# Optimization experiments

Hardware: AMD Instinct MI355X
Metric: run time of the kernel (lower is better)

Reference implementation:

```python
import jax, jax.numpy as jnp
import numpy as np
from jax import lax

L = 50      # observation_len
P = 30      # pred_len
N = 2048    # num nearby obstacles
EMB = 64    # embed_size
NH = 128    # node_hidden_size
EH = 256    # edge_hidden_size
AD = 64     # attention_dim
CNN = 2048  # resnet50 fc.in_features


def setup_inputs() -> dict:
    key = jax.random.key(0)
    ks = jax.random.split(key, 20)
    def rn(k, shape, s=1.0):
        return jax.random.normal(k, shape, jnp.float32) * s
    w = 0.05
    return {
        "img_embedding": rn(ks[0], (1, CNN)),
        "target_obs_pos": rn(ks[1], (1, L, 2)),
        "target_obs_pos_rel": rn(ks[2], (1, L, 2)),
        "nearby_obs_pos": rn(ks[3], (1, N, L, 2)),
        "nearby_obs_pos_rel": rn(ks[4], (1, N, L, 2)),
        "nearby_obs_hist_sizes": jax.random.randint(ks[5], (1, N, 1), 0, L + 1),
        "target_obs_hist_size": L,
        "target_h0": rn(ks[6], (NH,), w),
        "target_c0": rn(ks[7], (NH,), w),
        "W_temb": rn(ks[8], (2, EMB), w), "b_temb": jnp.zeros((EMB,), jnp.float32),
        "Wih_t": rn(ks[9], (EMB, 4 * NH), w), "Whh_t": rn(ks[10], (NH, 4 * NH), w),
        "bih_t": jnp.zeros((4 * NH,), jnp.float32), "bhh_t": jnp.zeros((4 * NH,), jnp.float32),
        "W_tatt": rn(ks[11], (2, AD), w), "b_tatt": jnp.zeros((AD,), jnp.float32),
        "nearby_h0": rn(ks[12], (EH,), w),
        "nearby_c0": rn(ks[13], (EH,), w),
        "W_nemb": rn(ks[14], (2, EMB), w), "b_nemb": jnp.zeros((EMB,), jnp.float32),
        "Wih_n": rn(ks[15], (EMB, 4 * EH), w), "Whh_n": rn(ks[16], (EH, 4 * EH), w),
        "bih_n": jnp.zeros((4 * EH,), jnp.float32), "bhh_n": jnp.zeros((4 * EH,), jnp.float32),
        "W_natt": rn(ks[17], (2, AD), w), "b_natt": jnp.zeros((AD,), jnp.float32),
        "W_pred": rn(ks[18], (NH + CNN + EH, 2), w), "b_pred": jnp.zeros((2,), jnp.float32),
    }


def _lstm_cell(x, h, c, Wih, Whh, bih, bhh, H):
    # PyTorch LSTM gate order: i, f, g, o
    g = x @ Wih + h @ Whh + bih + bhh
    i = jax.nn.sigmoid(g[..., :H])
    f = jax.nn.sigmoid(g[..., H:2 * H])
    gg = jnp.tanh(g[..., 2 * H:3 * H])
    o = jax.nn.sigmoid(g[..., 3 * H:])
    c2 = f * c + i * gg
    return o * jnp.tanh(c2), c2


def _forward(img_embedding, target_obs_pos, target_obs_pos_rel, nearby_obs_pos,
             nearby_obs_pos_rel, target_h0, target_c0, W_temb, b_temb,
             Wih_t, Whh_t, bih_t, bhh_t, W_tatt, b_tatt,
             nearby_h0, nearby_c0, W_nemb, b_nemb,
             Wih_n, Whh_n, bih_n, bhh_n, W_natt, b_natt,
             W_pred, b_pred, nearby_obs_hist_sizes, target_obs_hist_size):
    nhist = nearby_obs_hist_sizes.reshape(N)
    inv_sqrt_d = 1.0 / jnp.sqrt(jnp.float32(AD))

    def attention(trel, tpos, npos, nh, nmask, Ht_prev):
        # scores scaled by curr_N / sqrt(attention_dim), softmax over masked nearby.
        # max-subtracted softmax is mathematically identical to the original exp/sum.
        currN = jnp.sum(nmask.astype(jnp.float32))
        an = (tpos - npos) @ W_natt + b_natt          # [N, AD]
        at = trel @ W_tatt + b_tatt                   # [AD]
        scores = (an @ at) * currN * inv_sqrt_d       # [N]
        w = jax.nn.softmax(jnp.where(nmask, scores, -1e30))
        return jnp.where(currN >= 1.0, w @ nh, Ht_prev)

    def obs_step(carry, x):
        th, tc, nh, nc, Ht = carry
        t, tpos, trel, npos, nrel = x
        tmask = target_obs_hist_size > (L - t)
        nmask = nhist > (L - t)
        th2, tc2 = _lstm_cell(trel @ W_temb + b_temb, th, tc, Wih_t, Whh_t, bih_t, bhh_t, NH)
        th = jnp.where(tmask, th2, th)
        tc = jnp.where(tmask, tc2, tc)
        nh2, nc2 = _lstm_cell(nrel @ W_nemb + b_nemb, nh, nc, Wih_n, Whh_n, bih_n, bhh_n, EH)
        m = nmask[:, None]
        nh = jnp.where(m, nh2, nh)
        nc = jnp.where(m, nc2, nc)
        Ht = attention(trel, tpos, npos, nh, nmask, Ht)
        return (th, tc, nh, nc, Ht), None

    np_tm = jnp.swapaxes(nearby_obs_pos[0], 0, 1)      # [L, N, 2] time-major
    nr_tm = jnp.swapaxes(nearby_obs_pos_rel[0], 0, 1)
    xs = (jnp.arange(1, L), target_obs_pos[0, 1:], target_obs_pos_rel[0, 1:],
          np_tm[1:], nr_tm[1:])
    init = (target_h0, target_c0,
            jnp.broadcast_to(nearby_h0, (N, EH)),
            jnp.broadcast_to(nearby_c0, (N, EH)),
            nearby_h0)
    (th, tc, nh, nc, Ht), _ = lax.scan(obs_step, init, xs)

    # During prediction the original reuses nearby pos/rel from the last obs step.
    npos_last = nearby_obs_pos[0, :, L - 1, :]
    nrel_last = nearby_obs_pos_rel[0, :, L - 1, :]
    xn_last = nrel_last @ W_nemb + b_nemb
    all_mask = jnp.ones((N,), bool)

    def pred_step(carry, _):
        th, tc, nh, nc, Ht, pos = carry
        pred = jnp.concatenate([th, img_embedding[0], Ht]) @ W_pred + b_pred  # [2]
        pos = pos + pred
        th, tc = _lstm_cell(pred @ W_temb + b_temb, th, tc, Wih_t, Whh_t, bih_t, bhh_t, NH)
        nh, nc = _lstm_cell(xn_last, nh, nc, Wih_n, Whh_n, bih_n, bhh_n, EH)
        Ht = attention(pred, pos, npos_last, nh, all_mask, Ht)
        return (th, tc, nh, nc, Ht, pos), pred

    carry0 = (th, tc, nh, nc, Ht, target_obs_pos[0, L - 1])
    _, preds = lax.scan(pred_step, carry0, None, length=P)
    return preds[None]                                 # [1, P, 2]


def reference(img_embedding, target_obs_pos, target_obs_pos_rel, nearby_obs_pos,
              nearby_obs_pos_rel, nearby_obs_hist_sizes, target_obs_hist_size,
              target_h0, target_c0, W_temb, b_temb, Wih_t, Whh_t, bih_t, bhh_t,
              W_tatt, b_tatt, nearby_h0, nearby_c0, W_nemb, b_nemb,
              Wih_n, Whh_n, bih_n, bhh_n, W_natt, b_natt, W_pred, b_pred):
    return _forward(img_embedding, target_obs_pos, target_obs_pos_rel, nearby_obs_pos,
                    nearby_obs_pos_rel, target_h0, target_c0, W_temb, b_temb,
                    Wih_t, Whh_t, bih_t, bhh_t, W_tatt, b_tatt,
                    nearby_h0, nearby_c0, W_nemb, b_nemb,
                    Wih_n, Whh_n, bih_n, bhh_n, W_natt, b_natt,
                    W_pred, b_pred, nearby_obs_hist_sizes, target_obs_hist_size)
```

## Files before the change

### kernel.cpp

```cpp
#include <hip/hip_runtime.h>
#include <hip/hip_bf16.h>
#include <cstdint>

#define LH   50
#define PP   30
#define NAG  2048
#define NHID 128
#define EHID 256
#define ADIM 64
#define CNND 2048

typedef __attribute__((ext_vector_type(8))) short bf16x8;
typedef __attribute__((ext_vector_type(4))) float f32x4;

enum : int {
  WS_WT  = 0,
  WS_WHT = 131072,
  WS_WFN = 163840,
  WS_BFN = 165888,
  WS_WFT = 166912,
  WS_BFT = 167936,
  WS_TH  = 168448,
  WS_TC  = 168576,
  WS_W49 = 168704,
  WS_CN  = 170752,
  WS_Z   = 170756,
  WS_FLG = 293636,
  WS_HG  = 293892,
  WS_END = 556036
};

__device__ __forceinline__ float sigf(float x){ return 1.0f/(1.0f + __expf(-x)); }
__device__ __forceinline__ float tanhfast(float x){
  x = fminf(15.0f, fmaxf(-15.0f, x));
  float e = __expf(2.0f*x);
  return (e - 1.0f)/(e + 1.0f);
}
__device__ __forceinline__ float bfs(short s){
  return __uint_as_float(((unsigned)(unsigned short)s) << 16);
}
__device__ __forceinline__ void ast(unsigned* p, unsigned v){
  __hip_atomic_store(p, v, __ATOMIC_RELAXED, __HIP_MEMORY_SCOPE_AGENT);
}
__device__ __forceinline__ unsigned ald(const unsigned* p){
  return __hip_atomic_load(p, __ATOMIC_RELAXED, __HIP_MEMORY_SCOPE_AGENT);
}

__global__ void k_prep(const float* __restrict__ Whhn, const float* __restrict__ Whht,
                       const float* __restrict__ Wnemb, const float* __restrict__ bnemb,
                       const float* __restrict__ Wihn,  const float* __restrict__ bihn,
                       const float* __restrict__ bhhn,
                       const float* __restrict__ Wtemb, const float* __restrict__ btemb,
                       const float* __restrict__ Wiht,  const float* __restrict__ biht,
                       const float* __restrict__ bhht,
                       const float* __restrict__ trel,  const int* __restrict__ thsp,
                       const float* __restrict__ th0,   const float* __restrict__ tc0,
                       const float* __restrict__ tpos,  const float* __restrict__ npos,
                       const int* __restrict__ nhist,
                       const float* __restrict__ Wtatt, const float* __restrict__ btatt,
                       const float* __restrict__ Wnatt, const float* __restrict__ bnatt,
                       float* __restrict__ ws)
{
  __shared__ float ps[2304];
  const int b = blockIdx.x, tid = threadIdx.x;
  if (b < 256){
    float (*t)[33] = (float(*)[33])ps;
    __hip_bfloat16* WT = (__hip_bfloat16*)(ws + WS_WT);
    const int tx = tid & 31, ty = tid >> 5;
    const int j0 = (b & 31) << 5;
    const int c  = b >> 5;
    const int e0 = c << 5;
    #pragma unroll
    for (int r = 0; r < 4; ++r)
      t[ty + 8*r][tx] = Whhn[(e0 + ty + 8*r)*1024 + j0 + tx];
    __syncthreads();
    #pragma unroll
    for (int r = 0; r < 4; ++r)
      WT[c*32768 + r*8192 + (j0 + tx)*8 + ty] = __float2bfloat16(t[ty + 8*r][tx]);
  } else if (b == 256){
    for (int j = tid; j < 1024; j += 256){
      float a0=0.f, a1=0.f, ab=0.f;
      for (int k=0;k<64;k++){
        const float w = Wihn[k*1024 + j];
        a0 += Wnemb[k]*w; a1 += Wnemb[64+k]*w; ab += bnemb[k]*w;
      }
      ws[WS_WFN + j]        = a0;
      ws[WS_WFN + 1024 + j] = a1;
      ws[WS_BFN + j]        = ab + bihn[j] + bhhn[j];
    }
    for (int j = tid; j < 512; j += 256){
      float a0=0.f, a1=0.f, ab=0.f;
      for (int k=0;k<64;k++){
        const float w = Wiht[k*512 + j];
        a0 += Wtemb[k]*w; a1 += Wtemb[64+k]*w; ab += btemb[k]*w;
      }
      ws[WS_WFT + j]       = a0;
      ws[WS_WFT + 512 + j] = a1;
      ws[WS_BFT + j]       = ab + biht[j] + bhht[j];
    }
    __hip_bfloat16* WTt = (__hip_bfloat16*)(ws + WS_WHT);
    for (int j = tid; j < 512; j += 256)
      for (int k = 0; k < 128; ++k)
        WTt[j*128 + k] = __float2bfloat16(Whht[k*512 + j]);
    ast((unsigned*)(ws + WS_FLG) + tid, 0u);
  } else if (b == 257){
    float* hT  = ps;
    float* cT  = ps + 128;
    float* gT  = ps + 256;
    float* wfa = ps + 768;
    float* wfb = ps + 1280;
    float* bfT = ps + 1792;
    #pragma unroll
    for (int q = 0; q < 2; ++q){
      const int j = tid + q*256;
      float a0=0.f, a1=0.f, ab=0.f;
      for (int k=0;k<64;k++){
        const float w = Wiht[k*512 + j];
        a0 += Wtemb[k]*w; a1 += Wtemb[64+k]*w; ab += btemb[k]*w;
      }
      wfa[j] = a0; wfb[j] = a1; bfT[j] = ab + biht[j] + bhht[j];
    }
    if (tid < 128){ hT[tid] = th0[tid]; cT[tid] = tc0[tid]; }
    __syncthreads();
    const int ths = thsp[0];
    int t0 = 51 - ths; if (t0 < 1) t0 = 1;
    for (int t = t0; t < 50; ++t){
      const float x0 = trel[2*t], x1 = trel[2*t+1];
      #pragma unroll
      for (int q = 0; q < 2; ++q){
        const int j = tid + q*256;
        float acc = x0*wfa[j] + x1*wfb[j] + bfT[j];
        for (int k = 0; k < 128; ++k) acc += hT[k]*Whht[k*512 + j];
        gT[j] = acc;
      }
      __syncthreads();
      if (tid < 128){
        const float ig = sigf(gT[tid]),          fg = sigf(gT[128 + tid]);
        const float gg = tanhfast(gT[256 + tid]), og = sigf(gT[384 + tid]);
        const float c2 = fg*cT[tid] + ig*gg;
        cT[tid] = c2; hT[tid] = og*tanhfast(c2);
      }
      __syncthreads();
    }
    if (tid < 128){ ws[WS_TH + tid] = hT[tid]; ws[WS_TC + tid] = cT[tid]; }
  } else {
    float* at  = ps;
    float* red = ps + 64;
    float* uv  = ps + 320;
    const int t = LH - 1;
    const float tr0 = trel[2*t], tr1 = trel[2*t+1];
    const float tp0 = tpos[2*t], tp1 = tpos[2*t+1];
    if (tid < ADIM) at[tid] = tr0*Wtatt[tid] + tr1*Wtatt[ADIM+tid] + btatt[tid];
    int cnt = 0;
    #pragma unroll
    for (int i = 0; i < 8; ++i) cnt += (nhist[tid + 256*i] > (LH - t)) ? 1 : 0;
    red[tid] = (float)cnt;
    __syncthreads();
    if (tid == 0){
      float u0=0.f,u1=0.f,v=0.f;
      for (int k=0;k<ADIM;k++){ u0 += Wnatt[k]*at[k]; u1 += Wnatt[ADIM+k]*at[k]; v += bnatt[k]*at[k]; }
      uv[0]=u0; uv[1]=u1; uv[2]=v;
    }
    for (int s = 128; s > 0; s >>= 1){ if (tid < s) red[tid] += red[tid+s]; __syncthreads(); }
    const float currN = red[0];
    __syncthreads();
    const float u0 = uv[0], u1 = uv[1], v = uv[2];
    const float scale = currN * 0.125f;
    float sc[8]; float smax = -3.0e38f;
    #pragma unroll
    for (int i = 0; i < 8; ++i){
      const int n = tid + 256*i;
      const float p0 = npos[n*100 + 2*t], p1 = npos[n*100 + 2*t + 1];
      float s = scale * ((tp0-p0)*u0 + (tp1-p1)*u1 + v);
      s = (nhist[n] > (LH - t)) ? s : -1.0e30f;
      sc[i] = s; smax = fmaxf(smax, s);
    }
    red[tid] = smax; __syncthreads();
    for (int s = 128; s > 0; s >>= 1){ if (tid<s) red[tid] = fmaxf(red[tid], red[tid+s]); __syncthreads(); }
    smax = red[0]; __syncthreads();
    float ssum = 0.f;
    #pragma unroll
    for (int i = 0; i < 8; ++i){ sc[i] = __expf(sc[i]-smax); ssum += sc[i]; }
    red[tid] = ssum; __syncthreads();
    for (int s = 128; s > 0; s >>= 1){ if (tid<s) red[tid] += red[tid+s]; __syncthreads(); }
    const float inv = 1.0f / red[0];
    #pragma unroll
    for (int i = 0; i < 8; ++i) ws[WS_W49 + tid + 256*i] = sc[i]*inv;
    if (tid == 0) ws[WS_CN] = currN;
  }
}

__global__ __launch_bounds__(256, 1) void k_phaseA(
    const float* __restrict__ nh0, const float* __restrict__ nc0,
    const float* __restrict__ nrel, const int* __restrict__ nhist,
    const float* __restrict__ Wpred,
    float* __restrict__ ws)
{
  extern __shared__ char smem[];
  const int tid = threadIdx.x;
  const int wv = tid >> 6, lane = tid & 63;
  const int lhi = lane >> 4, llo = lane & 15;

  const int pb = blockIdx.x;
  const int agrp = pb & 127;
  const int h    = pb >> 7;
  const int pidx = pb ^ 128;
  const int n0   = agrp << 4;
  unsigned* flg = (unsigned*)(ws + WS_FLG);
  short* HgS = (short*)(ws + WS_HG);

  short* ldsW = (short*)smem;
  short* Hl   = (short*)(smem + 131072);
  float* relS = (float*)(smem + 139520);
  float* vS   = (float*)(smem + 145920);
  float* zS   = (float*)(smem + 147968);
  float* wfL  = (float*)(smem + 151808);
  const short* wt = (const short*)(ws + WS_WT);

  bf16x8 wreg[4][4][2];
  #pragma unroll
  for (int c = 0; c < 4; ++c)
    #pragma unroll
    for (int g = 0; g < 4; ++g)
      #pragma unroll
      for (int t = 0; t < 2; ++t){
        const int j = g*256 + h*128 + (wv<<5) + t*16 + llo;
        wreg[c][g][t] = *(const bf16x8*)(wt + c*32768 + lhi*8192 + j*8);
      }
  for (int u = tid; u < 8192; u += 256){
    const int lane_u = u & 63;
    const int t_u  = (u >> 6) & 1;
    const int g_u  = (u >> 7) & 3;
    const int wv_u = (u >> 9) & 3;
    const int c_u  = (u >> 11) & 3;
    const int llo_u = lane_u & 15, lhi_u = lane_u >> 4;
    const int j_u = g_u*256 + h*128 + wv_u*32 + t_u*16 + llo_u;
    *(uint4*)(ldsW + u*8) = *(const uint4*)(wt + (4+c_u)*32768 + lhi_u*8192 + j_u*8);
  }
  for (int i = tid; i < 512; i += 256){
    const int llo_i = i & 15, t_i = (i >> 4) & 1, g_i = (i >> 5) & 3, wv_i = (i >> 7) & 3;
    const int j = g_i*256 + h*128 + wv_i*32 + t_i*16 + llo_i;
    wfL[i]        = ws[WS_WFN + j];
    wfL[512 + i]  = ws[WS_WFN + 1024 + j];
    wfL[1024 + i] = ws[WS_BFN + j];
  }
  for (int i = tid; i < 1600; i += 256){
    const int a = i / 100, r = i % 100;
    relS[a*100 + r] = nrel[(n0 + a)*100 + r];
  }
  vS[2*tid]   = Wpred[2*(NHID + CNND + tid)];
  vS[2*tid+1] = Wpred[2*(NHID + CNND + tid) + 1];
  for (int i = tid; i < 4096; i += 256){
    const int a = i >> 8, e = i & 255;
    ((__hip_bfloat16*)Hl)[a*264 + e] = __float2bfloat16(nh0[e]);
  }
  float C[4][2];
  #pragma unroll
  for (int r = 0; r < 4; ++r)
    #pragma unroll
    for (int t = 0; t < 2; ++t)
      C[r][t] = nc0[h*128 + (wv<<5) + t*16 + llo];
  int nh4[4];
  #pragma unroll
  for (int r = 0; r < 4; ++r) nh4[r] = nhist[n0 + lhi*4 + r];
  int nhmax = 0;
  for (int a = 0; a < 16; ++a){ const int v = nhist[n0 + a]; nhmax = (v > nhmax) ? v : nhmax; }
  __syncthreads();

  for (int st = 1; st <= 78; ++st){
    const int thr  = (st <= 49) ? (50 - st) : -1;
    const int tsel = (st <= 49) ? st : 49;
    const bool skip = (nhmax <= thr);

    if (!skip){
      const short* hc = Hl + llo*264 + lhi*8;
      bf16x8 af[8];
      #pragma unroll
      for (int c = 0; c < 8; ++c) af[c] = *(const bf16x8*)(hc + c*32);

      f32x4 acc[4][2];
      #pragma unroll
      for (int g = 0; g < 4; ++g)
        #pragma unroll
        for (int t = 0; t < 2; ++t) acc[g][t] = (f32x4){0.f,0.f,0.f,0.f};

      #pragma unroll
      for (int c = 0; c < 4; ++c)
        #pragma unroll
        for (int g = 0; g < 4; ++g)
          #pragma unroll
          for (int t = 0; t < 2; ++t)
            acc[g][t] = __builtin_amdgcn_mfma_f32_16x16x32_bf16(af[c], wreg[c][g][t], acc[g][t], 0,0,0);
      #pragma unroll
      for (int c = 0; c < 4; ++c)
        #pragma unroll
        for (int g = 0; g < 4; ++g)
          #pragma unroll
          for (int t = 0; t < 2; ++t){
            const bf16x8 bw = *(const bf16x8*)(ldsW + (c*2048 + wv*512 + g*128 + t*64 + lane)*8);
            acc[g][t] = __builtin_amdgcn_mfma_f32_16x16x32_bf16(af[4+c], bw, acc[g][t], 0,0,0);
          }

      float2 rr[4];
      #pragma unroll
      for (int r = 0; r < 4; ++r)
        rr[r] = *(const float2*)(relS + (lhi*4 + r)*100 + 2*tsel);
      volatile float* wfv = wfL;
      short hpub[2][4];
      #pragma unroll
      for (int t = 0; t < 2; ++t){
        float wa[4], wb2[4], wbias[4];
        #pragma unroll
        for (int g = 0; g < 4; ++g){
          const int idx = ((wv*4 + g)*2 + t)*16 + llo;
          wa[g] = wfv[idx]; wb2[g] = wfv[512 + idx]; wbias[g] = wfv[1024 + idx];
        }
        const int e = h*128 + (wv<<5) + t*16 + llo;
        #pragma unroll
        for (int r = 0; r < 4; ++r){
          const float gi = acc[0][t][r] + rr[r].x*wa[0] + rr[r].y*wb2[0] + wbias[0];
          const float gf = acc[1][t][r] + rr[r].x*wa[1] + rr[r].y*wb2[1] + wbias[1];
          const float gg = acc[2][t][r] + rr[r].x*wa[2] + rr[r].y*wb2[2] + wbias[2];
          const float go = acc[3][t][r] + rr[r].x*wa[3] + rr[r].y*wb2[3] + wbias[3];
          const float c2 = sigf(gf)*C[r][t] + sigf(gi)*tanhfast(gg);
          const float h2 = sigf(go)*tanhfast(c2);
          const bool mk = nh4[r] > thr;
          if (mk) C[r][t] = c2;
          const short hold = Hl[(lhi*4 + r)*264 + e];
          short hnv; { __hip_bfloat16 hb = __float2bfloat16(h2); hnv = *(short*)&hb; }
          hpub[t][r] = mk ? hnv : hold;
        }
      }
      __syncthreads();
      #pragma unroll
      for (int t = 0; t < 2; ++t){
        const int e = h*128 + (wv<<5) + t*16 + llo;
        #pragma unroll
        for (int r = 0; r < 4; ++r)
          Hl[(lhi*4 + r)*264 + e] = hpub[t][r];
      }
      __syncthreads();
      {
        const int a = tid >> 4, i = tid & 15;
        const uint4 v = *(const uint4*)(Hl + a*264 + h*128 + i*8);
        unsigned* dst = (unsigned*)(HgS + (st & 1)*524288 + (n0 + a)*256 + h*128) + i*4;
        ast(dst+0, v.x); ast(dst+1, v.y); ast(dst+2, v.z); ast(dst+3, v.w);
      }
      __syncthreads();
      if (tid == 0){
        ast(&flg[pb], (unsigned)st);
        while ((int)ald(&flg[pidx]) < st) {}
      }
      __syncthreads();
      {
        const int a = tid >> 4, i = tid & 15;
        const unsigned* src = (const unsigned*)(HgS + (st & 1)*524288 + (n0 + a)*256 + (h^1)*128) + i*4;
        uint4 v;
        v.x = ald(src+0); v.y = ald(src+1); v.z = ald(src+2); v.w = ald(src+3);
        *(uint4*)(Hl + a*264 + (h^1)*128 + i*8) = v;
      }
      __syncthreads();
    } else {
      if (tid == 0) ast(&flg[pb], (unsigned)st);
    }

    if (st >= 49 && h == 0){
      const int s = st - 49;
      const int a = tid >> 4, sub = tid & 15;
      const short* hp = Hl + a*264 + sub*16;
      float z0 = 0.f, z1 = 0.f;
      #pragma unroll
      for (int i = 0; i < 16; ++i){
        const float hv = bfs(hp[i]);
        z0 += hv*vS[2*(sub*16 + i)];
        z1 += hv*vS[2*(sub*16 + i) + 1];
      }
      #pragma unroll
      for (int o = 8; o > 0; o >>= 1){
        z0 += __shfl_down(z0, o, 16);
        z1 += __shfl_down(z1, o, 16);
      }
      if (sub == 0){
        zS[s*32 + a*2]     = z0;
        zS[s*32 + a*2 + 1] = z1;
      }
    }
  }
  __syncthreads();
  if (h == 0){
    for (int i = tid; i < 960; i += 256){
      const int s = i >> 5, rem = i & 31;
      ws[WS_Z + (s*NAG + n0 + (rem >> 1))*2 + (rem & 1)] = zS[i];
    }
  }
}

template<int K>
__device__ __forceinline__ void bredN(const float* v, volatile float* scratch,
                                      volatile float* outv, int tid){
  const int lane = tid & 63, wv = tid >> 6;
  #pragma unroll
  for (int k = 0; k < K; ++k){
    float x = v[k];
    #pragma unroll
    for (int o = 32; o > 0; o >>= 1) x += __shfl_down(x, o, 64);
    if (lane == 0) scratch[k*8 + wv] = x;
  }
  __syncthreads();
  if (tid == 0){
    #pragma unroll
    for (int k = 0; k < K; ++k){
      float s = 0.f;
      for (int i = 0; i < 8; ++i) s += scratch[k*8 + i];
      outv[k] = s;
    }
  }
  __syncthreads();
}

__device__ __forceinline__ float bredMax1(float x, volatile float* scratch,
                                          volatile float* outv, int tid){
  const int lane = tid & 63, wv = tid >> 6;
  #pragma unroll
  for (int o = 32; o > 0; o >>= 1) x = fmaxf(x, __shfl_down(x, o, 64));
  if (lane == 0) scratch[wv] = x;
  __syncthreads();
  if (tid == 0){
    float s = -3.0e38f;
    for (int i = 0; i < 8; ++i) s = fmaxf(s, scratch[i]);
    outv[0] = s;
  }
  __syncthreads();
  return outv[0];
}

__global__ __launch_bounds__(512, 1) void k_phaseB(
    const float* __restrict__ img, const float* __restrict__ tpos,
    const float* __restrict__ npos, const float* __restrict__ nh0,
    const float* __restrict__ Wpred, const float* __restrict__ bpred,
    const float* __restrict__ Wtatt, const float* __restrict__ btatt,
    const float* __restrict__ Wnatt, const float* __restrict__ bnatt,
    float* __restrict__ ws, float* __restrict__ out)
{
  __shared__ float p0s[NAG], p1s[NAG];
  __shared__ float th[128], tc[128], gl[512], at[64];
  __shared__ float scratch[24];
  __shared__ float bc[8];
  const int tid = threadIdx.x, lane = tid & 63, wv = tid >> 6;

  bf16x8 wreg[16];
  {
    const short* wp = (const short*)(ws + WS_WHT) + tid*128;
    #pragma unroll
    for (int f = 0; f < 16; ++f) wreg[f] = *(const bf16x8*)(wp + f*8);
  }
  for (int n = tid; n < NAG; n += 512){
    p0s[n] = npos[n*100 + 98];
    p1s[n] = npos[n*100 + 99];
  }
  if (tid < 128){ th[tid] = ws[WS_TH + tid]; tc[tid] = ws[WS_TC + tid]; }

  {
    float v[2] = {0.f, 0.f};
    for (int k = tid; k < CNND; k += 512){
      v[0] += img[k]*Wpred[2*(128 + k)];
      v[1] += img[k]*Wpred[2*(128 + k) + 1];
    }
    bredN<2>(v, scratch, bc, tid);
  }
  const float imgW0 = bc[0], imgW1 = bc[1];
  {
    float v[2] = {0.f, 0.f};
    if (tid < 256){
      v[0] = nh0[tid]*Wpred[2*(128 + CNND + tid)];
      v[1] = nh0[tid]*Wpred[2*(128 + CNND + tid) + 1];
    }
    bredN<2>(v, scratch, bc + 2, tid);
  }
  const float fb0 = bc[2], fb1 = bc[3];
  const float currN = ws[WS_CN];
  float pos0 = tpos[98], pos1 = tpos[99];
  float u0 = 0.f, u1 = 0.f, A = 0.f;
  __syncthreads();

  for (int s = 0; s < PP; ++s){
    const float* zs = ws + WS_Z + s*(NAG*2);
    float hv0, hv1;
    if (s == 0){
      if (currN >= 1.0f){
        float v[2] = {0.f, 0.f};
        for (int n = tid; n < NAG; n += 512){
          const float w = ws[WS_W49 + n];
          v[0] += w*zs[2*n]; v[1] += w*zs[2*n + 1];
        }
        bredN<2>(v, scratch, bc, tid);
        hv0 = bc[0]; hv1 = bc[1];
      } else { hv0 = fb0; hv1 = fb1; }
    } else {
      float sc[4], mx = -3.0e38f;
      #pragma unroll
      for (int i = 0; i < 4; ++i){
        const int n = tid + 512*i;
        sc[i] = 256.0f * (A - (p0s[n]*u0 + p1s[n]*u1));
        mx = fmaxf(mx, sc[i]);
      }
      mx = bredMax1(mx, scratch, bc + 7, tid);
      float v[3] = {0.f, 0.f, 0.f};
      #pragma unroll
      for (int i = 0; i < 4; ++i){
        const int n = tid + 512*i;
        const float e = __expf(sc[i] - mx);
        v[0] += e; v[1] += e*zs[2*n]; v[2] += e*zs[2*n + 1];
      }
      bredN<3>(v, scratch, bc, tid);
      const float inv = 1.0f / bc[0];
      hv0 = bc[1]*inv; hv1 = bc[2]*inv;
    }
    {
      float v[2] = {0.f, 0.f};
      if (tid < 128){
        v[0] = th[tid]*Wpred[2*tid];
        v[1] = th[tid]*Wpred[2*tid + 1];
      }
      bredN<2>(v, scratch, bc + 2, tid);
    }
    const float pr0 = bc[2] + imgW0 + hv0 + bpred[0];
    const float pr1 = bc[3] + imgW1 + hv1 + bpred[1];
    if (tid == 0){ out[2*s] = pr0; out[2*s + 1] = pr1; }
    pos0 += pr0; pos1 += pr1;

    {
      float g = pr0*ws[WS_WFT + tid] + pr1*ws[WS_WFT + 512 + tid] + ws[WS_BFT + tid];
      #pragma unroll
      for (int f = 0; f < 16; ++f){
        #pragma unroll
        for (int i = 0; i < 8; ++i)
          g += bfs(wreg[f][i]) * th[f*8 + i];
      }
      gl[tid] = g;
    }
    __syncthreads();
    float hnew = 0.f, cnew = 0.f;
    if (tid < 128){
      const float ig = sigf(gl[tid]),           fg = sigf(gl[128 + tid]);
      const float gg = tanhfast(gl[256 + tid]), og = sigf(gl[384 + tid]);
      cnew = fg*tc[tid] + ig*gg;
      hnew = og*tanhfast(cnew);
    }
    __syncthreads();
    if (tid < 128){ th[tid] = hnew; tc[tid] = cnew; }

    if (tid < ADIM) at[tid] = pr0*Wtatt[tid] + pr1*Wtatt[ADIM + tid] + btatt[tid];
    __syncthreads();
    if (wv == 0){
      float uu0 = Wnatt[lane]*at[lane];
      float uu1 = Wnatt[ADIM + lane]*at[lane];
      float vv  = bnatt[lane]*at[lane];
      #pragma unroll
      for (int o = 32; o > 0; o >>= 1){
        uu0 += __shfl_down(uu0, o, 64);
        uu1 += __shfl_down(uu1, o, 64);
        vv  += __shfl_down(vv,  o, 64);
      }
      if (lane == 0){
        bc[4] = uu0; bc[5] = uu1;
        bc[6] = pos0*uu0 + pos1*uu1 + vv;
      }
    }
    __syncthreads();
    u0 = bc[4]; u1 = bc[5]; A = bc[6];
  }
}

extern "C" void kernel_launch(void* const* d_in, const int* in_sizes, int n_in,
                              void* d_out, int out_size, void* d_ws, size_t ws_size,
                              hipStream_t stream) {
  const float* img   = (const float*)d_in[0];
  const float* tpos  = (const float*)d_in[1];
  const float* trel  = (const float*)d_in[2];
  const float* npos  = (const float*)d_in[3];
  const float* nrel  = (const float*)d_in[4];
  const int*   nhist = (const int*)d_in[5];
  const int*   ths   = (const int*)d_in[6];
  const float* th0   = (const float*)d_in[7];
  const float* tc0   = (const float*)d_in[8];
  const float* Wtemb = (const float*)d_in[9];
  const float* btemb = (const float*)d_in[10];
  const float* Wiht  = (const float*)d_in[11];
  const float* Whht  = (const float*)d_in[12];
  const float* biht  = (const float*)d_in[13];
  const float* bhht  = (const float*)d_in[14];
  const float* Wtatt = (const float*)d_in[15];
  const float* btatt = (const float*)d_in[16];
  const float* nh0   = (const float*)d_in[17];
  const float* nc0   = (const float*)d_in[18];
  const float* Wnemb = (const float*)d_in[19];
  const float* bnemb = (const float*)d_in[20];
  const float* Wihn  = (const float*)d_in[21];
  const float* Whhn  = (const float*)d_in[22];
  const float* bihn  = (const float*)d_in[23];
  const float* bhhn  = (const float*)d_in[24];
  const float* Wnatt = (const float*)d_in[25];
  const float* bnatt = (const float*)d_in[26];
  const float* Wpred = (const float*)d_in[27];
  const float* bpred = (const float*)d_in[28];
  float* ws  = (float*)d_ws;
  float* out = (float*)d_out;

  const int ldsA = 157952;

  k_prep<<<259, 256, 0, stream>>>(Whhn, Whht, Wnemb, bnemb, Wihn, bihn, bhhn,
                                  Wtemb, btemb, Wiht, biht, bhht,
                                  trel, ths, th0, tc0, tpos, npos, nhist,
                                  Wtatt, btatt, Wnatt, bnatt, ws);
  k_phaseA<<<256, 256, ldsA, stream>>>(nh0, nc0, nrel, nhist, Wpred, ws);
  k_phaseB<<<1, 512, 0, stream>>>(img, tpos, npos, nh0, Wpred, bpred,
                                  Wtatt, btatt, Wnatt, bnatt, ws, out);
}
```

Before: 840.9 us.

## Split z projection across halves, vectorize cross-block h exchange, fuse reductions

```diff
diff --git a/kernel.cpp b/kernel.cpp
--- a/kernel.cpp
+++ b/kernel.cpp
@@ -9,9 +9,11 @@
 #define EHID 256
 #define ADIM 64
 #define CNND 2048
+#define ZHALF 122880
 
 typedef __attribute__((ext_vector_type(8))) short bf16x8;
 typedef __attribute__((ext_vector_type(4))) float f32x4;
+typedef __attribute__((ext_vector_type(4))) unsigned u32x4;
 
 enum : int {
   WS_WT  = 0,
@@ -25,9 +27,9 @@
   WS_W49 = 168704,
   WS_CN  = 170752,
   WS_Z   = 170756,
-  WS_FLG = 293636,
-  WS_HG  = 293892,
-  WS_END = 556036
+  WS_FLG = 416516,
+  WS_HG  = 416772,
+  WS_END = 678916
 };
 
 __device__ __forceinline__ float sigf(float x){ return 1.0f/(1.0f + __expf(-x)); }
@@ -44,6 +46,14 @@
 }
 __device__ __forceinline__ unsigned ald(const unsigned* p){
   return __hip_atomic_load(p, __ATOMIC_RELAXED, __HIP_MEMORY_SCOPE_AGENT);
+}
+__device__ __forceinline__ void stg16(void* p, u32x4 v){
+  asm volatile("global_store_dwordx4 %0, %1, off sc0 sc1" :: "v"(p), "v"(v) : "memory");
+}
+__device__ __forceinline__ u32x4 ldg16(const void* p){
+  u32x4 v;
+  asm volatile("global_load_dwordx4 %0, %1, off sc0 sc1" : "=v"(v) : "v"(p) : "memory");
+  return v;
 }
 
 __global__ void k_prep(const float* __restrict__ Whhn, const float* __restrict__ Whht,
@@ -340,58 +350,63 @@
           Hl[(lhi*4 + r)*264 + e] = hpub[t][r];
       }
       __syncthreads();
+    }
+
+    if (st >= 49){
+      const int s = st - 49;
+      const int a = tid >> 4, sub = tid & 15;
+      const int e0 = h*128 + sub*8;
+      const short* hp = Hl + a*264 + e0;
+      float z0 = 0.f, z1 = 0.f;
+      #pragma unroll
+      for (int i = 0; i < 8; ++i){
+        const float hv = bfs(hp[i]);
+        z0 += hv*vS[2*(e0 + i)];
+        z1 += hv*vS[2*(e0 + i) + 1];
+      }
+      #pragma unroll
+      for (int o = 8; o > 0; o >>= 1){
+        z0 += __shfl_down(z0, o, 16);
+        z1 += __shfl_down(z1, o, 16);
+      }
+      if (sub == 0){
+        zS[s*32 + a*2]     = z0;
+        zS[s*32 + a*2 + 1] = z1;
+      }
+    }
+
+    if (!skip && st < 78){
       {
         const int a = tid >> 4, i = tid & 15;
-        const uint4 v = *(const uint4*)(Hl + a*264 + h*128 + i*8);
-        unsigned* dst = (unsigned*)(HgS + (st & 1)*524288 + (n0 + a)*256 + h*128) + i*4;
-        ast(dst+0, v.x); ast(dst+1, v.y); ast(dst+2, v.z); ast(dst+3, v.w);
-      }
-      __syncthreads();
+        const u32x4 v = *(const u32x4*)(Hl + a*264 + h*128 + i*8);
+        stg16(HgS + (st & 1)*524288 + (n0 + a)*256 + h*128 + i*8, v);
+      }
+      asm volatile("s_waitcnt vmcnt(0)" ::: "memory");
+      __builtin_amdgcn_sched_barrier(0);
+      __builtin_amdgcn_s_barrier();
+      __builtin_amdgcn_sched_barrier(0);
       if (tid == 0){
         ast(&flg[pb], (unsigned)st);
         while ((int)ald(&flg[pidx]) < st) {}
       }
-      __syncthreads();
+      __builtin_amdgcn_sched_barrier(0);
+      __builtin_amdgcn_s_barrier();
+      __builtin_amdgcn_sched_barrier(0);
       {
         const int a = tid >> 4, i = tid & 15;
-        const unsigned* src = (const unsigned*)(HgS + (st & 1)*524288 + (n0 + a)*256 + (h^1)*128) + i*4;
-        uint4 v;
-        v.x = ald(src+0); v.y = ald(src+1); v.z = ald(src+2); v.w = ald(src+3);
-        *(uint4*)(Hl + a*264 + (h^1)*128 + i*8) = v;
+        u32x4 v = ldg16(HgS + (st & 1)*524288 + (n0 + a)*256 + (h^1)*128 + i*8);
+        asm volatile("s_waitcnt vmcnt(0)" ::: "memory");
+        __builtin_amdgcn_sched_barrier(0);
+        *(u32x4*)(Hl + a*264 + (h^1)*128 + i*8) = v;
       }
       __syncthreads();
-    } else {
-      if (tid == 0) ast(&flg[pb], (unsigned)st);
-    }
-
-    if (st >= 49 && h == 0){
-      const int s = st - 49;
-      const int a = tid >> 4, sub = tid & 15;
-      const short* hp = Hl + a*264 + sub*16;
-      float z0 = 0.f, z1 = 0.f;
-      #pragma unroll
-      for (int i = 0; i < 16; ++i){
-        const float hv = bfs(hp[i]);
-        z0 += hv*vS[2*(sub*16 + i)];
-        z1 += hv*vS[2*(sub*16 + i) + 1];
-      }
-      #pragma unroll
-      for (int o = 8; o > 0; o >>= 1){
-        z0 += __shfl_down(z0, o, 16);
-        z1 += __shfl_down(z1, o, 16);
-      }
-      if (sub == 0){
-        zS[s*32 + a*2]     = z0;
-        zS[s*32 + a*2 + 1] = z1;
-      }
     }
   }
   __syncthreads();
-  if (h == 0){
-    for (int i = tid; i < 960; i += 256){
-      const int s = i >> 5, rem = i & 31;
-      ws[WS_Z + (s*NAG + n0 + (rem >> 1))*2 + (rem & 1)] = zS[i];
-    }
+  for (int i = tid; i < 960; i += 256){
+    const int s = i >> 5, rem = i & 31;
+    const int a = rem >> 1, comp = rem & 1;
+    ws[WS_Z + h*ZHALF + (s*2 + comp)*NAG + n0 + a] = zS[i];
   }
 }
 
@@ -423,11 +438,11 @@
   const int lane = tid & 63, wv = tid >> 6;
   #pragma unroll
   for (int o = 32; o > 0; o >>= 1) x = fmaxf(x, __shfl_down(x, o, 64));
-  if (lane == 0) scratch[wv] = x;
+  if (lane == 0) scratch[40 + wv] = x;
   __syncthreads();
   if (tid == 0){
     float s = -3.0e38f;
-    for (int i = 0; i < 8; ++i) s = fmaxf(s, scratch[i]);
+    for (int i = 0; i < 8; ++i) s = fmaxf(s, scratch[40 + i]);
     outv[0] = s;
   }
   __syncthreads();
@@ -444,8 +459,10 @@
 {
   __shared__ float p0s[NAG], p1s[NAG];
   __shared__ float th[128], tc[128], gl[512], at[64];
-  __shared__ float scratch[24];
+  __shared__ float scratch[48];
   __shared__ float bc[8];
+  __shared__ float uab[3];
+  __shared__ float pv[4];
   const int tid = threadIdx.x, lane = tid & 63, wv = tid >> 6;
 
   bf16x8 wreg[16];
@@ -479,23 +496,32 @@
   }
   const float fb0 = bc[2], fb1 = bc[3];
   const float currN = ws[WS_CN];
+  const float bp0 = bpred[0], bp1 = bpred[1];
   float pos0 = tpos[98], pos1 = tpos[99];
   float u0 = 0.f, u1 = 0.f, A = 0.f;
   __syncthreads();
 
   for (int s = 0; s < PP; ++s){
-    const float* zs = ws + WS_Z + s*(NAG*2);
-    float hv0, hv1;
+    const float* zb = ws + WS_Z + (s*2)*NAG;
+    float pr0, pr1;
     if (s == 0){
+      float v[4] = {0.f, 0.f, 0.f, 0.f};
       if (currN >= 1.0f){
-        float v[2] = {0.f, 0.f};
         for (int n = tid; n < NAG; n += 512){
           const float w = ws[WS_W49 + n];
-          v[0] += w*zs[2*n]; v[1] += w*zs[2*n + 1];
+          v[0] += w*(zb[n] + zb[ZHALF + n]);
+          v[1] += w*(zb[NAG + n] + zb[ZHALF + NAG + n]);
         }
-        bredN<2>(v, scratch, bc, tid);
-        hv0 = bc[0]; hv1 = bc[1];
-      } else { hv0 = fb0; hv1 = fb1; }
+      }
+      if (tid < 128){
+        v[2] = th[tid]*Wpred[2*tid];
+        v[3] = th[tid]*Wpred[2*tid + 1];
+      }
+      bredN<4>(v, scratch, bc, tid);
+      const float hv0 = (currN >= 1.0f) ? bc[0] : fb0;
+      const float hv1 = (currN >= 1.0f) ? bc[1] : fb1;
+      pr0 = bc[2] + imgW0 + hv0 + bp0;
+      pr1 = bc[3] + imgW1 + hv1 + bp1;
     } else {
       float sc[4], mx = -3.0e38f;
       #pragma unroll
@@ -505,30 +531,29 @@
         mx = fmaxf(mx, sc[i]);
       }
       mx = bredMax1(mx, scratch, bc + 7, tid);
-      float v[3] = {0.f, 0.f, 0.f};
+      float v[5] = {0.f, 0.f, 0.f, 0.f, 0.f};
       #pragma unroll
       for (int i = 0; i < 4; ++i){
         const int n = tid + 512*i;
         const float e = __expf(sc[i] - mx);
-        v[0] += e; v[1] += e*zs[2*n]; v[2] += e*zs[2*n + 1];
-      }
-      bredN<3>(v, scratch, bc, tid);
+        v[0] += e;
+        v[1] += e*(zb[n] + zb[ZHALF + n]);
+        v[2] += e*(zb[NAG + n] + zb[ZHALF + NAG + n]);
+      }
+      if (tid < 128){
+        v[3] = th[tid]*Wpred[2*tid];
+        v[4] = th[tid]*Wpred[2*tid + 1];
+      }
+      bredN<5>(v, scratch, bc, tid);
       const float inv = 1.0f / bc[0];
-      hv0 = bc[1]*inv; hv1 = bc[2]*inv;
-    }
-    {
-      float v[2] = {0.f, 0.f};
-      if (tid < 128){
-        v[0] = th[tid]*Wpred[2*tid];
-        v[1] = th[tid]*Wpred[2*tid + 1];
-      }
-      bredN<2>(v, scratch, bc + 2, tid);
-    }
-    const float pr0 = bc[2] + imgW0 + hv0 + bpred[0];
-    const float pr1 = bc[3] + imgW1 + hv1 + bpred[1];
-    if (tid == 0){ out[2*s] = pr0; out[2*s + 1] = pr1; }
-    pos0 += pr0; pos1 += pr1;
-
+      pr0 = bc[3] + imgW0 + bc[1]*inv + bp0;
+      pr1 = bc[4] + imgW1 + bc[2]*inv + bp1;
+    }
+    if (tid == 0){
+      out[2*s] = pr0; out[2*s + 1] = pr1;
+      pos0 += pr0; pos1 += pr1;
+      pv[2] = pos0; pv[3] = pos1;
+    }
     {
       float g = pr0*ws[WS_WFT + tid] + pr1*ws[WS_WFT + 512 + tid] + ws[WS_BFT + tid];
       #pragma unroll
@@ -539,20 +564,15 @@
       }
       gl[tid] = g;
     }
+    if (tid < ADIM) at[tid] = pr0*Wtatt[tid] + pr1*Wtatt[ADIM + tid] + btatt[tid];
     __syncthreads();
-    float hnew = 0.f, cnew = 0.f;
     if (tid < 128){
       const float ig = sigf(gl[tid]),           fg = sigf(gl[128 + tid]);
       const float gg = tanhfast(gl[256 + tid]), og = sigf(gl[384 + tid]);
-      cnew = fg*tc[tid] + ig*gg;
-      hnew = og*tanhfast(cnew);
-    }
-    __syncthreads();
-    if (tid < 128){ th[tid] = hnew; tc[tid] = cnew; }
-
-    if (tid < ADIM) at[tid] = pr0*Wtatt[tid] + pr1*Wtatt[ADIM + tid] + btatt[tid];
-    __syncthreads();
-    if (wv == 0){
+      const float cnew = fg*tc[tid] + ig*gg;
+      tc[tid] = cnew;
+      th[tid] = og*tanhfast(cnew);
+    } else if (wv == 7){
       float uu0 = Wnatt[lane]*at[lane];
       float uu1 = Wnatt[ADIM + lane]*at[lane];
       float vv  = bnatt[lane]*at[lane];
@@ -563,12 +583,12 @@
         vv  += __shfl_down(vv,  o, 64);
       }
       if (lane == 0){
-        bc[4] = uu0; bc[5] = uu1;
-        bc[6] = pos0*uu0 + pos1*uu1 + vv;
+        uab[0] = uu0; uab[1] = uu1;
+        uab[2] = pv[2]*uu0 + pv[3]*uu1 + vv;
       }
     }
     __syncthreads();
-    u0 = bc[4]; u1 = bc[5]; A = bc[6];
+    u0 = uab[0]; u1 = uab[1]; A = uab[2];
   }
 }
 
```

After: 900.1 us. +7.0%, slower.
